# Kernel tuning notes

Measured on AMD Instinct MI355X. Metric: run time of the kernel, lower is better.

Reference implementation:

```python
import jax, jax.numpy as jnp
from jax import lax
import numpy as np

B, T, A = 8192, 512, 4  # sessions, trials, n_actions


def setup_inputs() -> dict:
    key = jax.random.key(0)
    k1, k2, k3 = jax.random.split(key, 3)
    choices = jax.random.randint(k1, (B, T), 0, A)
    actions = jax.nn.one_hot(choices, A, dtype=jnp.float32)          # one-hot actions
    rew = (jax.random.uniform(k2, (B, T)) < 0.5).astype(jnp.float32)  # binary rewards
    rewards = jnp.broadcast_to(rew[..., None], (B, T, A))
    inputs = jnp.concatenate([actions, rewards], axis=-1)            # [B,T,2A]
    params_raw = jax.random.normal(k3, (13,), jnp.float32) * 0.5
    return {"inputs": inputs, "params_raw": params_raw}


def _transform(p):
    sp, sg = jax.nn.softplus, jax.nn.sigmoid
    return dict(
        beta_r=jnp.clip(sp(p[0]), 0.01, 20.0),
        lapse=jnp.clip(sg(p[1]), 0.01, 0.99),
        prior=jnp.clip(sp(p[2]), 0.01, 0.99),
        alpha=jnp.clip(sg(p[3]), 0.01, 0.99),
        decay=jnp.clip(sg(p[4]), 0.01, 0.99),
        ab1=p[5], ab2=p[6],
        pers=sp(p[7]), sw=p[8],
        gamma=sp(p[10]),
        temp=jnp.clip(sp(p[11]) + 1e-6, 1e-6, 100.0),
        beta_p=sp(p[12]),
    )


def _forward(inputs, params_raw):
    pr = _transform(params_raw)
    nb = inputs.shape[0]
    actions_t = jnp.swapaxes(inputs[..., :A], 0, 1)   # [T,B,A]
    rewards_t = jnp.swapaxes(inputs[..., A:2 * A], 0, 1)

    q0 = jnp.ones((nb, A), jnp.float32) * pr["prior"]
    old0 = jnp.full((nb,), -1, jnp.int32)
    tsls0 = jnp.zeros((nb,), jnp.float32)
    expl0 = jnp.full((nb,), 1.0, jnp.float32) * pr["alpha"]
    cum0 = jnp.zeros((nb, A), jnp.float32)

    def step(carry, xr):
        q, old, tsls, expl, cum = carry
        a, r = xr
        cc = jnp.argmax(a, axis=-1).astype(jnp.int32)          # current choice
        oh = jax.nn.one_hot(cc, A, dtype=q.dtype)
        rv = jnp.sum(r * a, axis=-1)                            # reward value
        delta = rv - pr["gamma"] * (1.0 - rv) - jnp.sum(q * oh, axis=-1)
        q = q + delta[:, None] * oh                             # Q update (full overwrite of error)
        same = cc == old
        tsls = jnp.where(same, tsls + 1.0, 0.0)
        expl = expl * (1.0 - 1e-3)                              # exploration decay
        cum = cum + oh
        qm = jnp.mean(q, axis=-1, keepdims=True)
        q = (1.0 - expl[:, None]) * q + expl[:, None] * qm      # mean-mixing exploration
        q = q * pr["decay"]
        probs = (1.0 - pr["lapse"]) * jax.nn.softmax(
            pr["beta_r"] * q / pr["temp"] + pr["beta_p"] * jnp.log1p(cum), axis=-1
        ) + pr["lapse"] / A
        logits = jnp.log(probs)
        oh_old = jax.nn.one_hot(old, A, dtype=q.dtype)          # zeros when old == -1
        bonus = (
            (jnp.where(same, pr["pers"], pr["sw"]))[:, None] * oh
            + pr["ab1"] * oh_old
            + pr["ab2"] * jax.nn.one_hot((cc + 2) % A, A, dtype=q.dtype)
            + oh * jnp.log(tsls + 1.0)[:, None]
        )
        return (q, cc, tsls, expl, cum), logits + bonus

    _, logits_t = lax.scan(step, (q0, old0, tsls0, expl0, cum0), (actions_t, rewards_t))
    return jnp.swapaxes(logits_t, 0, 1)  # [B,T,A]


def reference(inputs, params_raw):
    return _forward(inputs, params_raw)
```

## Files before the change

### kernel.cpp

```cpp
#include <hip/hip_runtime.h>
#include <math.h>

constexpr int B_ = 8192;
constexpr int T_ = 512;
constexpr int CH = 16;
constexpr int NCH = T_ / CH;
constexpr int GRPS = B_ / 64;
constexpr int ROWB = CH * 16 + 16;
constexpr size_t PACK_BYTES = (size_t)B_ * T_;
constexpr size_t SN = (size_t)GRPS * NCH * 64;
constexpr size_t SNAP_BYTES = SN * 3 * sizeof(float4);

__device__ __forceinline__ float sp_(float x) {
    return fmaxf(x, 0.0f) + log1pf(expf(-fabsf(x)));
}
__device__ __forceinline__ float sg_(float x) { return 1.0f / (1.0f + expf(-x)); }
__device__ __forceinline__ float clipf(float x, float lo, float hi) { return fminf(fmaxf(x, lo), hi); }
__device__ __forceinline__ float sel(bool c, float a, float b) { return c ? a : b; }

struct CS { float q0, q1, q2, q3, c0, c1, c2, c3, tsls, expl; int oldc; };

__device__ __forceinline__ void step_carry(CS& s, unsigned int byte, float gamma, float decay,
                                           bool& same, bool& i0, bool& i1, bool& i2, bool& i3,
                                           int& cc_out) {
    const int  cc = (int)(byte & 3u);
    const bool rf = (byte & 4u) != 0u;
    const float target = sel(rf, 1.0f, -gamma);
    same = (cc == s.oldc);
    s.tsls = sel(same, s.tsls + 1.0f, 0.0f);
    s.expl *= (1.0f - 1e-3f);
    i0 = (cc == 0); i1 = (cc == 1); i2 = (cc == 2); i3 = (cc == 3);
    s.q0 = sel(i0, target, s.q0);  s.c0 += sel(i0, 1.0f, 0.0f);
    s.q1 = sel(i1, target, s.q1);  s.c1 += sel(i1, 1.0f, 0.0f);
    s.q2 = sel(i2, target, s.q2);  s.c2 += sel(i2, 1.0f, 0.0f);
    s.q3 = sel(i3, target, s.q3);  s.c3 += sel(i3, 1.0f, 0.0f);
    const float qm  = 0.25f * ((s.q0 + s.q1) + (s.q2 + s.q3));
    const float omd = (1.0f - s.expl) * decay;
    const float eqd = (s.expl * decay) * qm;
    s.q0 = fmaf(omd, s.q0, eqd);
    s.q1 = fmaf(omd, s.q1, eqd);
    s.q2 = fmaf(omd, s.q2, eqd);
    s.q3 = fmaf(omd, s.q3, eqd);
    s.oldc = cc;
    cc_out = cc;
}


__global__ __launch_bounds__(256) void pack_kernel(const float* __restrict__ in,
                                                   unsigned char* __restrict__ pk) {
    const int tid  = blockIdx.x * 256 + threadIdx.x;
    const int ti   = tid & 15;
    const int lane = (tid >> 4) & 63;
    const int tile = (tid >> 10) & (NCH - 1);
    const int grp  = tid >> 15;
    const int b = (grp << 6) | lane;
    const int t = (tile << 4) | ti;
    const float* base = in + ((size_t)b * T_ + t) * 8;
    const float4 a = *reinterpret_cast<const float4*>(base);
    const float  r = base[4];
    const int cc = a.y > 0.5f ? 1 : (a.z > 0.5f ? 2 : (a.w > 0.5f ? 3 : 0));
    pk[tid] = (unsigned char)(cc | ((r > 0.5f) ? 4 : 0));
}

__global__ __launch_bounds__(256) void scan_snap(const unsigned char* __restrict__ pk,
                                                 const float* __restrict__ p,
                                                 float4* __restrict__ snap4) {
    const int tid  = threadIdx.x;
    const int w    = tid >> 6;
    const int lane = tid & 63;
    const int k    = lane & 31;
    const int b    = blockIdx.x * 8 + w * 2 + (lane >> 5);
    const int grp  = b >> 6;
    const int sl   = b & 63;

    const float prior = clipf(sp_(p[2]), 0.01f, 0.99f);
    const float alpha = clipf(sg_(p[3]), 0.01f, 0.99f);
    const float decay = clipf(sg_(p[4]), 0.01f, 0.99f);
    const float gamma = sp_(p[10]);

    const float e0k = alpha * __powf(1.0f - 1e-3f, (float)(CH * k));

    const uint4 cw = reinterpret_cast<const uint4*>(pk)[(size_t)(grp * NCH + k) * 64 + sl];

    float m[4][4], v[4], n[4];
#pragma unroll
    for (int i = 0; i < 4; ++i) {
#pragma unroll
        for (int j = 0; j < 4; ++j) m[i][j] = (i == j) ? 1.0f : 0.0f;
        v[i] = 0.0f; n[i] = 0.0f;
    }
    int prev = -1, run = 0;
    float e = e0k;

#pragma unroll
    for (int ti = 0; ti < CH; ++ti) {
        const unsigned word = (ti < 4) ? cw.x : (ti < 8) ? cw.y : (ti < 12) ? cw.z : cw.w;
        const unsigned byte = (word >> (8 * (ti & 3))) & 0xffu;
        const int  cc = (int)(byte & 3u);
        const bool rf = (byte & 4u) != 0u;
        const float tgt = rf ? 1.0f : -gamma;
        e *= (1.0f - 1e-3f);
        run = (cc == prev) ? (run + 1) : 1;
        prev = cc;
#pragma unroll
        for (int i = 0; i < 4; ++i) {
            const bool hit = (i == cc);
            v[i] = hit ? tgt : v[i];
            n[i] += hit ? 1.0f : 0.0f;
#pragma unroll
            for (int j = 0; j < 4; ++j) m[i][j] = hit ? 0.0f : m[i][j];
        }
        const float aa = decay * (1.0f - e);
        const float bf = decay * e * 0.25f;
        float csum[4];
#pragma unroll
        for (int j = 0; j < 4; ++j) csum[j] = bf * ((m[0][j] + m[1][j]) + (m[2][j] + m[3][j]));
        const float vs = bf * ((v[0] + v[1]) + (v[2] + v[3]));
#pragma unroll
        for (int i = 0; i < 4; ++i) {
#pragma unroll
            for (int j = 0; j < 4; ++j) m[i][j] = fmaf(aa, m[i][j], csum[j]);
            v[i] = fmaf(aa, v[i], vs);
        }
    }

    float sm[4][4], sv[4];
#pragma unroll
    for (int i = 0; i < 4; ++i) {
#pragma unroll
        for (int j = 0; j < 4; ++j) sm[i][j] = m[i][j];
        sv[i] = v[i];
    }
#pragma unroll
    for (int d = 1; d < 32; d <<= 1) {
        float pm[4][4], pv[4];
#pragma unroll
        for (int i = 0; i < 4; ++i) {
#pragma unroll
            for (int j = 0; j < 4; ++j) pm[i][j] = __shfl_up(sm[i][j], d, 32);
            pv[i] = __shfl_up(sv[i], d, 32);
        }
        if (k >= d) {
            float nm[4][4], nv[4];
#pragma unroll
            for (int i = 0; i < 4; ++i) {
#pragma unroll
                for (int j = 0; j < 4; ++j)
                    nm[i][j] = fmaf(sm[i][0], pm[0][j], fmaf(sm[i][1], pm[1][j],
                               fmaf(sm[i][2], pm[2][j], sm[i][3] * pm[3][j])));
                nv[i] = fmaf(sm[i][0], pv[0], fmaf(sm[i][1], pv[1],
                        fmaf(sm[i][2], pv[2], fmaf(sm[i][3], pv[3], sv[i]))));
            }
#pragma unroll
            for (int i = 0; i < 4; ++i) {
#pragma unroll
                for (int j = 0; j < 4; ++j) sm[i][j] = nm[i][j];
                sv[i] = nv[i];
            }
        }
    }

    float q[4];
#pragma unroll
    for (int i = 0; i < 4; ++i) {
        float er0 = __shfl_up(sm[i][0], 1, 32);
        float er1 = __shfl_up(sm[i][1], 1, 32);
        float er2 = __shfl_up(sm[i][2], 1, 32);
        float er3 = __shfl_up(sm[i][3], 1, 32);
        float ev  = __shfl_up(sv[i], 1, 32);
        if (k == 0) { er0 = (i == 0); er1 = (i == 1); er2 = (i == 2); er3 = (i == 3); ev = 0.0f; }
        q[i] = fmaf(prior, ((er0 + er1) + (er2 + er3)), ev);
    }

    float cex[4];
#pragma unroll
    for (int i = 0; i < 4; ++i) {
        float s = n[i];
#pragma unroll
        for (int d = 1; d < 32; d <<= 1) {
            const float t = __shfl_up(s, d, 32);
            if (k >= d) s += t;
        }
        cex[i] = s - n[i];
    }

    const float lcf  = (float)prev;
    const float runf = (float)run;
    float lcm1 = __shfl_up(lcf, 1, 32);
    if (k == 0) lcm1 = -1.0f;
    const bool u = (runf == 16.0f) && (lcf == lcm1);
    const unsigned long long bal = __ballot(u);
    const unsigned gm = (unsigned)(bal >> (lane & 32));
    const unsigned vsh = (k == 31) ? gm : (gm << (31 - k));
    const int c = __clz(~vsh);
    const float runsrc = __shfl(runf, (lane & 32) + (k - c));
    const float TR = 16.0f * (float)c + runsrc;
    float TRm1 = __shfl_up(TR, 1, 32);
    const float tsls = (k == 0) ? 0.0f : (TRm1 - 1.0f);
    const float lcprev = (k == 0) ? -1.0f : lcm1;

    const size_t sb = (size_t)(grp * NCH + k) * 64 + sl;
    snap4[0 * SN + sb] = make_float4(q[0], q[1], q[2], q[3]);
    snap4[1 * SN + sb] = make_float4(cex[0], cex[1], cex[2], cex[3]);
    snap4[2 * SN + sb] = make_float4(tsls, e0k, lcprev, 0.0f);
}

__global__ __launch_bounds__(64) void chunk_logits(const unsigned char* __restrict__ pk,
                                                   const float* __restrict__ p,
                                                   const float4* __restrict__ snap4,
                                                   float* __restrict__ out) {
    __shared__ unsigned char lds[64 * ROWB];
    const int l   = threadIdx.x;
    const int bid = blockIdx.x;
    const int k   = bid & (NCH - 1);
    const int grp = bid >> 5;

    const float beta_r = clipf(sp_(p[0]), 0.01f, 20.0f);
    const float lapse  = clipf(sg_(p[1]), 0.01f, 0.99f);
    const float decay  = clipf(sg_(p[4]), 0.01f, 0.99f);
    const float ab1    = p[5];
    const float ab2    = p[6];
    const float pers   = sp_(p[7]);
    const float sw     = p[8];
    const float gamma  = sp_(p[10]);
    const float temp   = clipf(sp_(p[11]) + 1e-6f, 1e-6f, 100.0f);
    const float beta_p = sp_(p[12]);
    const float brt = beta_r / temp;
    const float l4  = lapse * 0.25f;
    const float oml = 1.0f - lapse;

    const size_t sb = (size_t)bid * 64 + l;
    const float4 qv = snap4[0 * SN + sb];
    const float4 cv = snap4[1 * SN + sb];
    const float4 mv = snap4[2 * SN + sb];
    CS s;
    s.q0 = qv.x; s.q1 = qv.y; s.q2 = qv.z; s.q3 = qv.w;
    s.c0 = cv.x; s.c1 = cv.y; s.c2 = cv.z; s.c3 = cv.w;
    s.tsls = mv.x; s.expl = mv.y; s.oldc = (int)mv.z;

    const uint4 cur = reinterpret_cast<const uint4*>(pk)[(size_t)bid * 64 + l];

#pragma unroll
    for (int ti = 0; ti < CH; ++ti) {
        const unsigned int word = (ti < 4) ? cur.x : (ti < 8) ? cur.y : (ti < 12) ? cur.z : cur.w;
        const unsigned int byte = (word >> (8 * (ti & 3))) & 0xffu;
        const int prev = s.oldc;
        bool same, i0, i1, i2, i3; int cc;
        step_carry(s, byte, gamma, decay, same, i0, i1, i2, i3, cc);

        const float s0 = fmaf(brt, s.q0, beta_p * __logf(1.0f + s.c0));
        const float s1 = fmaf(brt, s.q1, beta_p * __logf(1.0f + s.c1));
        const float s2 = fmaf(brt, s.q2, beta_p * __logf(1.0f + s.c2));
        const float s3 = fmaf(brt, s.q3, beta_p * __logf(1.0f + s.c3));
        const float m  = fmaxf(fmaxf(s0, s1), fmaxf(s2, s3));
        const float e0 = __expf(s0 - m);
        const float e1 = __expf(s1 - m);
        const float e2 = __expf(s2 - m);
        const float e3 = __expf(s3 - m);
        const float iz = oml / ((e0 + e1) + (e2 + e3));

        float l0 = __logf(fmaf(e0, iz, l4));
        float l1 = __logf(fmaf(e1, iz, l4));
        float l2 = __logf(fmaf(e2, iz, l4));
        float l3 = __logf(fmaf(e3, iz, l4));

        const float bcc = sel(same, pers, sw) + __logf(s.tsls + 1.0f);
        const int cc2 = cc ^ 2;
        l0 += sel(i0, bcc, 0.0f) + sel(prev == 0, ab1, 0.0f) + sel(cc2 == 0, ab2, 0.0f);
        l1 += sel(i1, bcc, 0.0f) + sel(prev == 1, ab1, 0.0f) + sel(cc2 == 1, ab2, 0.0f);
        l2 += sel(i2, bcc, 0.0f) + sel(prev == 2, ab1, 0.0f) + sel(cc2 == 2, ab2, 0.0f);
        l3 += sel(i3, bcc, 0.0f) + sel(prev == 3, ab1, 0.0f) + sel(cc2 == 3, ab2, 0.0f);

        *reinterpret_cast<float4*>(&lds[l * ROWB + ti * 16]) = make_float4(l0, l1, l2, l3);
    }

    __syncthreads();
    float4* __restrict__ out4 = reinterpret_cast<float4*>(out);
#pragma unroll
    for (int pp = 0; pp < 16; ++pp) {
        const int ss = pp * 4 + (l >> 4);
        const int st = l & 15;
        const float4 v = *reinterpret_cast<const float4*>(&lds[ss * ROWB + st * 16]);
        out4[((size_t)(grp * 64 + ss)) * T_ + k * CH + st] = v;
    }
}


__global__ __launch_bounds__(64, 1) void castro_scan_packed(
    const unsigned char* __restrict__ pk, const float* __restrict__ p, float* __restrict__ out)
{
    __shared__ unsigned char lds[64 * ROWB];
    const int l = threadIdx.x, blk = blockIdx.x;
    const float beta_r = clipf(sp_(p[0]), 0.01f, 20.0f);
    const float lapse  = clipf(sg_(p[1]), 0.01f, 0.99f);
    const float prior  = clipf(sp_(p[2]), 0.01f, 0.99f);
    const float alpha  = clipf(sg_(p[3]), 0.01f, 0.99f);
    const float decay  = clipf(sg_(p[4]), 0.01f, 0.99f);
    const float ab1 = p[5], ab2 = p[6];
    const float pers = sp_(p[7]), sw = p[8];
    const float gamma = sp_(p[10]);
    const float temp = clipf(sp_(p[11]) + 1e-6f, 1e-6f, 100.0f);
    const float beta_p = sp_(p[12]);
    const float brt = beta_r / temp, l4 = lapse * 0.25f, oml = 1.0f - lapse;
    CS s; s.q0 = s.q1 = s.q2 = s.q3 = prior;
    s.c0 = s.c1 = s.c2 = s.c3 = 0.0f; s.tsls = 0.0f; s.expl = alpha; s.oldc = -1;
    const uint4* pkt = reinterpret_cast<const uint4*>(pk + (size_t)blk * (NCH * 1024)) + l;
    float4* out4 = reinterpret_cast<float4*>(out);
    uint4 cur = pkt[0];
    for (int k = 0; k < NCH; ++k) {
        const uint4 nxt = pkt[(k + 1 < NCH ? k + 1 : k) * 64];
#pragma unroll
        for (int ti = 0; ti < CH; ++ti) {
            const unsigned int word = (ti < 4) ? cur.x : (ti < 8) ? cur.y : (ti < 12) ? cur.z : cur.w;
            const unsigned int byte = (word >> (8 * (ti & 3))) & 0xffu;
            const int prev = s.oldc;
            bool same, i0, i1, i2, i3; int cc;
            step_carry(s, byte, gamma, decay, same, i0, i1, i2, i3, cc);
            const float s0 = fmaf(brt, s.q0, beta_p * __logf(1.0f + s.c0));
            const float s1 = fmaf(brt, s.q1, beta_p * __logf(1.0f + s.c1));
            const float s2 = fmaf(brt, s.q2, beta_p * __logf(1.0f + s.c2));
            const float s3 = fmaf(brt, s.q3, beta_p * __logf(1.0f + s.c3));
            const float m = fmaxf(fmaxf(s0, s1), fmaxf(s2, s3));
            const float e0 = __expf(s0 - m), e1 = __expf(s1 - m);
            const float e2 = __expf(s2 - m), e3 = __expf(s3 - m);
            const float iz = oml / ((e0 + e1) + (e2 + e3));
            float l0 = __logf(fmaf(e0, iz, l4)), l1 = __logf(fmaf(e1, iz, l4));
            float l2 = __logf(fmaf(e2, iz, l4)), l3 = __logf(fmaf(e3, iz, l4));
            const float bcc = sel(same, pers, sw) + __logf(s.tsls + 1.0f);
            const int cc2 = cc ^ 2;
            l0 += sel(i0, bcc, 0.f) + sel(prev == 0, ab1, 0.f) + sel(cc2 == 0, ab2, 0.f);
            l1 += sel(i1, bcc, 0.f) + sel(prev == 1, ab1, 0.f) + sel(cc2 == 1, ab2, 0.f);
            l2 += sel(i2, bcc, 0.f) + sel(prev == 2, ab1, 0.f) + sel(cc2 == 2, ab2, 0.f);
            l3 += sel(i3, bcc, 0.f) + sel(prev == 3, ab1, 0.f) + sel(cc2 == 3, ab2, 0.f);
            *reinterpret_cast<float4*>(&lds[l * ROWB + ti * 16]) = make_float4(l0, l1, l2, l3);
        }
        __syncthreads();
#pragma unroll
        for (int pp = 0; pp < 16; ++pp) {
            const int ss = pp * 4 + (l >> 4);
            const int st = l & 15;
            const float4 v = *reinterpret_cast<const float4*>(&lds[ss * ROWB + st * 16]);
            out4[((size_t)(blk * 64 + ss)) * T_ + k * CH + st] = v;
        }
        __syncthreads();
        cur = nxt;
    }
}

extern "C" void kernel_launch(void* const* d_in, const int* in_sizes, int n_in,
                              void* d_out, int out_size, void* d_ws, size_t ws_size,
                              hipStream_t stream) {
    const float* inputs = (const float*)d_in[0];
    const float* params = (const float*)d_in[1];
    float* out = (float*)d_out;

    if (ws_size >= PACK_BYTES + SNAP_BYTES) {
        unsigned char* pk = (unsigned char*)d_ws;
        float4* snap4 = (float4*)((char*)d_ws + PACK_BYTES);
        pack_kernel<<<dim3((B_ * T_) / 256), dim3(256), 0, stream>>>(inputs, pk);
        scan_snap<<<dim3(B_ / 8), dim3(256), 0, stream>>>(pk, params, snap4);
        chunk_logits<<<dim3(GRPS * NCH), dim3(64), 0, stream>>>(pk, params, snap4, out);
    } else if (ws_size >= PACK_BYTES) {
        unsigned char* pk = (unsigned char*)d_ws;
        pack_kernel<<<dim3((B_ * T_) / 256), dim3(256), 0, stream>>>(inputs, pk);
        castro_scan_packed<<<dim3(GRPS), dim3(64), 0, stream>>>(pk, params, out);
    }
}
```

Before: 87.83 us.

## Fuse chunk scan and logits into one kernel, drop snapshot round-trip

Result: faster. 79.35 us (-9.6%).

```diff
diff --git a/kernel.cpp b/kernel.cpp
--- a/kernel.cpp
+++ b/kernel.cpp
@@ -8,8 +8,6 @@
 constexpr int GRPS = B_ / 64;
 constexpr int ROWB = CH * 16 + 16;
 constexpr size_t PACK_BYTES = (size_t)B_ * T_;
-constexpr size_t SN = (size_t)GRPS * NCH * 64;
-constexpr size_t SNAP_BYTES = SN * 3 * sizeof(float4);
 
 __device__ __forceinline__ float sp_(float x) {
     return fmaxf(x, 0.0f) + log1pf(expf(-fabsf(x)));
@@ -62,21 +60,36 @@
     pk[tid] = (unsigned char)(cc | ((r > 0.5f) ? 4 : 0));
 }
 
-__global__ __launch_bounds__(256) void scan_snap(const unsigned char* __restrict__ pk,
-                                                 const float* __restrict__ p,
-                                                 float4* __restrict__ snap4) {
+__global__ __launch_bounds__(256, 4) void fused_scan_logits(const unsigned char* __restrict__ pk,
+                                                            const float* __restrict__ p,
+                                                            float* __restrict__ out) {
+    __shared__ float4 stg[8][8][33];
+
     const int tid  = threadIdx.x;
     const int w    = tid >> 6;
     const int lane = tid & 63;
     const int k    = lane & 31;
-    const int b    = blockIdx.x * 8 + w * 2 + (lane >> 5);
+    const int sess = w * 2 + (lane >> 5);
+    const int b0   = blockIdx.x * 8;
+    const int b    = b0 + sess;
     const int grp  = b >> 6;
     const int sl   = b & 63;
 
-    const float prior = clipf(sp_(p[2]), 0.01f, 0.99f);
-    const float alpha = clipf(sg_(p[3]), 0.01f, 0.99f);
-    const float decay = clipf(sg_(p[4]), 0.01f, 0.99f);
-    const float gamma = sp_(p[10]);
+    const float beta_r = clipf(sp_(p[0]), 0.01f, 20.0f);
+    const float lapse  = clipf(sg_(p[1]), 0.01f, 0.99f);
+    const float prior  = clipf(sp_(p[2]), 0.01f, 0.99f);
+    const float alpha  = clipf(sg_(p[3]), 0.01f, 0.99f);
+    const float decay  = clipf(sg_(p[4]), 0.01f, 0.99f);
+    const float ab1    = p[5];
+    const float ab2    = p[6];
+    const float pers   = sp_(p[7]);
+    const float sw     = p[8];
+    const float gamma  = sp_(p[10]);
+    const float temp   = clipf(sp_(p[11]) + 1e-6f, 1e-6f, 100.0f);
+    const float beta_p = sp_(p[12]);
+    const float brt = beta_r / temp;
+    const float l4  = lapse * 0.25f;
+    const float oml = 1.0f - lapse;
 
     const float e0k = alpha * __powf(1.0f - 1e-3f, (float)(CH * k));
 
@@ -196,92 +209,82 @@
     const float runsrc = __shfl(runf, (lane & 32) + (k - c));
     const float TR = 16.0f * (float)c + runsrc;
     float TRm1 = __shfl_up(TR, 1, 32);
-    const float tsls = (k == 0) ? 0.0f : (TRm1 - 1.0f);
+    const float tslsS = (k == 0) ? 0.0f : (TRm1 - 1.0f);
     const float lcprev = (k == 0) ? -1.0f : lcm1;
 
-    const size_t sb = (size_t)(grp * NCH + k) * 64 + sl;
-    snap4[0 * SN + sb] = make_float4(q[0], q[1], q[2], q[3]);
-    snap4[1 * SN + sb] = make_float4(cex[0], cex[1], cex[2], cex[3]);
-    snap4[2 * SN + sb] = make_float4(tsls, e0k, lcprev, 0.0f);
-}
-
-__global__ __launch_bounds__(64) void chunk_logits(const unsigned char* __restrict__ pk,
-                                                   const float* __restrict__ p,
-                                                   const float4* __restrict__ snap4,
-                                                   float* __restrict__ out) {
-    __shared__ unsigned char lds[64 * ROWB];
-    const int l   = threadIdx.x;
-    const int bid = blockIdx.x;
-    const int k   = bid & (NCH - 1);
-    const int grp = bid >> 5;
-
-    const float beta_r = clipf(sp_(p[0]), 0.01f, 20.0f);
-    const float lapse  = clipf(sg_(p[1]), 0.01f, 0.99f);
-    const float decay  = clipf(sg_(p[4]), 0.01f, 0.99f);
-    const float ab1    = p[5];
-    const float ab2    = p[6];
-    const float pers   = sp_(p[7]);
-    const float sw     = p[8];
-    const float gamma  = sp_(p[10]);
-    const float temp   = clipf(sp_(p[11]) + 1e-6f, 1e-6f, 100.0f);
-    const float beta_p = sp_(p[12]);
-    const float brt = beta_r / temp;
-    const float l4  = lapse * 0.25f;
-    const float oml = 1.0f - lapse;
-
-    const size_t sb = (size_t)bid * 64 + l;
-    const float4 qv = snap4[0 * SN + sb];
-    const float4 cv = snap4[1 * SN + sb];
-    const float4 mv = snap4[2 * SN + sb];
-    CS s;
-    s.q0 = qv.x; s.q1 = qv.y; s.q2 = qv.z; s.q3 = qv.w;
-    s.c0 = cv.x; s.c1 = cv.y; s.c2 = cv.z; s.c3 = cv.w;
-    s.tsls = mv.x; s.expl = mv.y; s.oldc = (int)mv.z;
-
-    const uint4 cur = reinterpret_cast<const uint4*>(pk)[(size_t)bid * 64 + l];
-
-#pragma unroll
-    for (int ti = 0; ti < CH; ++ti) {
-        const unsigned int word = (ti < 4) ? cur.x : (ti < 8) ? cur.y : (ti < 12) ? cur.z : cur.w;
-        const unsigned int byte = (word >> (8 * (ti & 3))) & 0xffu;
-        const int prev = s.oldc;
-        bool same, i0, i1, i2, i3; int cc;
-        step_carry(s, byte, gamma, decay, same, i0, i1, i2, i3, cc);
-
-        const float s0 = fmaf(brt, s.q0, beta_p * __logf(1.0f + s.c0));
-        const float s1 = fmaf(brt, s.q1, beta_p * __logf(1.0f + s.c1));
-        const float s2 = fmaf(brt, s.q2, beta_p * __logf(1.0f + s.c2));
-        const float s3 = fmaf(brt, s.q3, beta_p * __logf(1.0f + s.c3));
-        const float m  = fmaxf(fmaxf(s0, s1), fmaxf(s2, s3));
-        const float e0 = __expf(s0 - m);
-        const float e1 = __expf(s1 - m);
-        const float e2 = __expf(s2 - m);
-        const float e3 = __expf(s3 - m);
-        const float iz = oml / ((e0 + e1) + (e2 + e3));
-
-        float l0 = __logf(fmaf(e0, iz, l4));
-        float l1 = __logf(fmaf(e1, iz, l4));
-        float l2 = __logf(fmaf(e2, iz, l4));
-        float l3 = __logf(fmaf(e3, iz, l4));
-
-        const float bcc = sel(same, pers, sw) + __logf(s.tsls + 1.0f);
-        const int cc2 = cc ^ 2;
-        l0 += sel(i0, bcc, 0.0f) + sel(prev == 0, ab1, 0.0f) + sel(cc2 == 0, ab2, 0.0f);
-        l1 += sel(i1, bcc, 0.0f) + sel(prev == 1, ab1, 0.0f) + sel(cc2 == 1, ab2, 0.0f);
-        l2 += sel(i2, bcc, 0.0f) + sel(prev == 2, ab1, 0.0f) + sel(cc2 == 2, ab2, 0.0f);
-        l3 += sel(i3, bcc, 0.0f) + sel(prev == 3, ab1, 0.0f) + sel(cc2 == 3, ab2, 0.0f);
-
-        *reinterpret_cast<float4*>(&lds[l * ROWB + ti * 16]) = make_float4(l0, l1, l2, l3);
-    }
-
-    __syncthreads();
+    float q0 = q[0], q1 = q[1], q2 = q[2], q3 = q[3];
+    float c0 = cex[0], c1 = cex[1], c2 = cex[2], c3 = cex[3];
+    float tsls = tslsS;
+    float expl = e0k;
+    int oldc = (int)lcprev;
+
     float4* __restrict__ out4 = reinterpret_cast<float4*>(out);
-#pragma unroll
-    for (int pp = 0; pp < 16; ++pp) {
-        const int ss = pp * 4 + (l >> 4);
-        const int st = l & 15;
-        const float4 v = *reinterpret_cast<const float4*>(&lds[ss * ROWB + st * 16]);
-        out4[((size_t)(grp * 64 + ss)) * T_ + k * CH + st] = v;
+
+#pragma unroll
+    for (int h = 0; h < 2; ++h) {
+#pragma unroll
+        for (int tl = 0; tl < 8; ++tl) {
+            const int ti = h * 8 + tl;
+            const unsigned word = (ti < 4) ? cw.x : (ti < 8) ? cw.y : (ti < 12) ? cw.z : cw.w;
+            const unsigned byte = (word >> (8 * (ti & 3))) & 0xffu;
+            const int  cc = (int)(byte & 3u);
+            const bool rf = (byte & 4u) != 0u;
+            const float target = sel(rf, 1.0f, -gamma);
+            const int prv = oldc;
+            const bool same = (cc == oldc);
+            tsls = sel(same, tsls + 1.0f, 0.0f);
+            expl *= (1.0f - 1e-3f);
+            const bool i0 = (cc == 0), i1 = (cc == 1), i2 = (cc == 2), i3 = (cc == 3);
+            q0 = sel(i0, target, q0);  c0 += sel(i0, 1.0f, 0.0f);
+            q1 = sel(i1, target, q1);  c1 += sel(i1, 1.0f, 0.0f);
+            q2 = sel(i2, target, q2);  c2 += sel(i2, 1.0f, 0.0f);
+            q3 = sel(i3, target, q3);  c3 += sel(i3, 1.0f, 0.0f);
+            const float qm  = 0.25f * ((q0 + q1) + (q2 + q3));
+            const float omd = (1.0f - expl) * decay;
+            const float eqd = (expl * decay) * qm;
+            q0 = fmaf(omd, q0, eqd);
+            q1 = fmaf(omd, q1, eqd);
+            q2 = fmaf(omd, q2, eqd);
+            q3 = fmaf(omd, q3, eqd);
+            oldc = cc;
+
+            const float s0 = fmaf(brt, q0, beta_p * __logf(1.0f + c0));
+            const float s1 = fmaf(brt, q1, beta_p * __logf(1.0f + c1));
+            const float s2 = fmaf(brt, q2, beta_p * __logf(1.0f + c2));
+            const float s3 = fmaf(brt, q3, beta_p * __logf(1.0f + c3));
+            const float mx = fmaxf(fmaxf(s0, s1), fmaxf(s2, s3));
+            const float e0 = __expf(s0 - mx);
+            const float e1 = __expf(s1 - mx);
+            const float e2 = __expf(s2 - mx);
+            const float e3 = __expf(s3 - mx);
+            const float iz = oml / ((e0 + e1) + (e2 + e3));
+
+            float l0 = __logf(fmaf(e0, iz, l4));
+            float l1 = __logf(fmaf(e1, iz, l4));
+            float l2 = __logf(fmaf(e2, iz, l4));
+            float l3 = __logf(fmaf(e3, iz, l4));
+
+            const float bcc = sel(same, pers, sw) + __logf(tsls + 1.0f);
+            const int cc2 = cc ^ 2;
+            l0 += sel(i0, bcc, 0.0f) + sel(prv == 0, ab1, 0.0f) + sel(cc2 == 0, ab2, 0.0f);
+            l1 += sel(i1, bcc, 0.0f) + sel(prv == 1, ab1, 0.0f) + sel(cc2 == 1, ab2, 0.0f);
+            l2 += sel(i2, bcc, 0.0f) + sel(prv == 2, ab1, 0.0f) + sel(cc2 == 2, ab2, 0.0f);
+            l3 += sel(i3, bcc, 0.0f) + sel(prv == 3, ab1, 0.0f) + sel(cc2 == 3, ab2, 0.0f);
+
+            stg[sess][tl][k] = make_float4(l0, l1, l2, l3);
+        }
+
+        __syncthreads();
+#pragma unroll
+        for (int j = 0; j < 8; ++j) {
+            const int s  = tid >> 5;
+            const int ee = j * 32 + (tid & 31);
+            const int kk = ee >> 3;
+            const int tl = ee & 7;
+            const float4 val = stg[s][tl][kk];
+            out4[(size_t)(b0 + s) * T_ + kk * CH + h * 8 + tl] = val;
+        }
+        __syncthreads();
     }
 }
 
@@ -354,15 +357,9 @@
     const float* params = (const float*)d_in[1];
     float* out = (float*)d_out;
 
-    if (ws_size >= PACK_BYTES + SNAP_BYTES) {
-        unsigned char* pk = (unsigned char*)d_ws;
-        float4* snap4 = (float4*)((char*)d_ws + PACK_BYTES);
-        pack_kernel<<<dim3((B_ * T_) / 256), dim3(256), 0, stream>>>(inputs, pk);
-        scan_snap<<<dim3(B_ / 8), dim3(256), 0, stream>>>(pk, params, snap4);
-        chunk_logits<<<dim3(GRPS * NCH), dim3(64), 0, stream>>>(pk, params, snap4, out);
-    } else if (ws_size >= PACK_BYTES) {
+    if (ws_size >= PACK_BYTES) {
         unsigned char* pk = (unsigned char*)d_ws;
         pack_kernel<<<dim3((B_ * T_) / 256), dim3(256), 0, stream>>>(inputs, pk);
-        castro_scan_packed<<<dim3(GRPS), dim3(64), 0, stream>>>(pk, params, out);
-    }
-}
+        fused_scan_logits<<<dim3(B_ / 8), dim3(256), 0, stream>>>(pk, params, out);
+    }
+}
```
